# Kernel optimization log

Measured on AMD Instinct MI355X. Metric: run time of the kernel, lower is better.

Reference implementation:

```python
import jax, jax.numpy as jnp
import numpy as np

N = 50000      # n_nodes
E = 800000     # edges (before self-loops)
IN = 128       # in_dim
HID = 32       # hidden_dim (per-head out channels)
HEADS = 4
EMB = 128      # embed_dim
LAYERS = 3
NEG_SLOPE = 0.2  # PyG GATv2 default leaky_relu slope


def _layer_norm(x, g, b):
    mu = jnp.mean(x, axis=-1, keepdims=True)
    var = jnp.var(x, axis=-1, keepdims=True)
    return g * (x - mu) / jnp.sqrt(var + 1e-5) + b


def _gatv2(h, src, dst, n, Wl, bl, Wr, br, att, bias):
    # GATv2Conv (PyG semantics, share_weights=False, concat=True).
    H, C = att.shape
    xl = (h @ Wl + bl).reshape(n, H, C)   # target (i) transform
    xr = (h @ Wr + br).reshape(n, H, C)   # source (j) transform
    x_i = xl[dst]                          # [Etot, H, C] gather
    x_j = xr[src]
    e = jax.nn.leaky_relu(x_i + x_j, NEG_SLOPE)
    logit = jnp.einsum('ehc,hc->eh', e, att)          # [Etot, H]
    # segment softmax over destination node (every node has a self-loop)
    m = jax.ops.segment_max(logit, dst, num_segments=n)
    ex = jnp.exp(logit - m[dst])
    den = jax.ops.segment_sum(ex, dst, num_segments=n)
    alpha = ex / (den[dst] + 1e-16)
    out = jax.ops.segment_sum(alpha[..., None] * x_j, dst, num_segments=n)
    return out.reshape(n, H * C) + bias


def setup_inputs() -> dict:
    key = jax.random.key(0)
    ks = iter(jax.random.split(key, 64))
    d = {}
    d['x'] = jax.random.normal(next(ks), (N, IN), jnp.float32)
    d['edge_index'] = jax.random.randint(next(ks), (2, E), 0, N, dtype=jnp.int64)

    def w(shape, fan):
        return jax.random.normal(next(ks), shape, jnp.float32) / np.float32(np.sqrt(fan))

    HC = HID * HEADS
    d['W_in'] = w((IN, HID), IN); d['b_in'] = jnp.zeros((HID,), jnp.float32)
    for i in range(LAYERS):
        ic = HID if i == 0 else HC
        d[f'Wl{i}'] = w((ic, HC), ic); d[f'bl{i}'] = jnp.zeros((HC,), jnp.float32)
        d[f'Wr{i}'] = w((ic, HC), ic); d[f'br{i}'] = jnp.zeros((HC,), jnp.float32)
        d[f'att{i}'] = w((HEADS, HID), HID)
        d[f'bo{i}'] = jnp.zeros((HC,), jnp.float32)
        d[f'g{i}'] = jnp.ones((HC,), jnp.float32)
        d[f'be{i}'] = jnp.zeros((HC,), jnp.float32)
    d['W_out'] = w((HC, EMB), HC); d['b_out'] = jnp.zeros((EMB,), jnp.float32)
    return d


def reference(x, edge_index, W_in, b_in,
              Wl0, bl0, Wr0, br0, att0, bo0, g0, be0,
              Wl1, bl1, Wr1, br1, att1, bo1, g1, be1,
              Wl2, bl2, Wr2, br2, att2, bo2, g2, be2,
              W_out, b_out):
    n = x.shape[0]
    loops = jnp.arange(n, dtype=edge_index.dtype)  # add_self_loops=True
    src = jnp.concatenate([edge_index[0], loops])
    dst = jnp.concatenate([edge_index[1], loops])

    h = jax.nn.gelu(x @ W_in + b_in, approximate=False)
    layers = [(Wl0, bl0, Wr0, br0, att0, bo0, g0, be0),
              (Wl1, bl1, Wr1, br1, att1, bo1, g1, be1),
              (Wl2, bl2, Wr2, br2, att2, bo2, g2, be2)]
    for (Wl, bl, Wr, br, att, bo, g, be) in layers:
        h_new = jax.nn.gelu(_layer_norm(_gatv2(h, src, dst, n, Wl, bl, Wr, br, att, bo), g, be), approximate=False)
        h = h + h_new if h.shape == h_new.shape else h_new  # dropout = identity (eval)
    out = h @ W_out + b_out
    norm = jnp.maximum(jnp.linalg.norm(out, axis=-1, keepdims=True), 1e-12)
    return out / norm
```

## Files before the change

kernel.cpp:

```cpp
#include <hip/hip_runtime.h>
#include <hip/hip_bf16.h>
#include <math.h>

#define N_NODES 50000
#define N_EDGES 800000
#define IN_DIM  128
#define HC_DIM  128
#define HID_C   32
#define SCAN_NB 196

typedef __attribute__((ext_vector_type(8))) short short8;
typedef __attribute__((ext_vector_type(4))) short short4v;
typedef __attribute__((ext_vector_type(4))) float f32x4;

__device__ __forceinline__ float gelu_f(float x){
    return 0.5f*x*(1.0f + erff(x*0.7071067811865475f));
}

__device__ __forceinline__ void split2(float f, short& h, short& l){
    __hip_bfloat16 bh = __float2bfloat16(f);
    float r = f - __bfloat162float(bh);
    __hip_bfloat16 blo = __float2bfloat16(r);
    h = *reinterpret_cast<short*>(&bh);
    l = *reinterpret_cast<short*>(&blo);
}

__global__ __launch_bounds__(256) void k_count(const int* __restrict__ dst, int* __restrict__ cnt){
    int e = blockIdx.x*256 + threadIdx.x;
    if(e<N_EDGES) atomicAdd(&cnt[dst[e]], 1);
}

__global__ __launch_bounds__(256) void k_scan1(const int* __restrict__ cnt, int* __restrict__ rowptr,
                                               int* __restrict__ part){
    __shared__ int sh[256];
    int t=threadIdx.x; int i=blockIdx.x*256+t;
    int v = (i<N_NODES)? cnt[i] : 0;
    sh[t]=v; __syncthreads();
    for(int off=1; off<256; off<<=1){
        int y = (t>=off)? sh[t-off] : 0;
        __syncthreads();
        sh[t] += y;
        __syncthreads();
    }
    if(i<N_NODES) rowptr[i] = sh[t]-v;
    if(t==255) part[blockIdx.x] = sh[255];
}

__global__ __launch_bounds__(256) void k_scan2(int* __restrict__ part){
    __shared__ int sh[256];
    int t=threadIdx.x;
    int v = (t<SCAN_NB)? part[t] : 0;
    sh[t]=v; __syncthreads();
    for(int off=1; off<256; off<<=1){
        int y=(t>=off)? sh[t-off]:0;
        __syncthreads();
        sh[t]+=y;
        __syncthreads();
    }
    if(t<SCAN_NB) part[t] = sh[t]-v;
}

__global__ __launch_bounds__(256) void k_scan3(int* __restrict__ rowptr, const int* __restrict__ part,
                                               int* __restrict__ cur){
    int t=threadIdx.x; int i=blockIdx.x*256+t;
    if(i<N_NODES){
        int v = rowptr[i] + part[blockIdx.x];
        rowptr[i]=v; cur[i]=v;
    }
    if(i==0) rowptr[N_NODES]=N_EDGES;
}

__global__ __launch_bounds__(256) void k_fill(const int* __restrict__ src, const int* __restrict__ dst,
                                              int* __restrict__ cur, int* __restrict__ col){
    int e = blockIdx.x*256+threadIdx.x;
    if(e<N_EDGES){
        int d = dst[e];
        int p = atomicAdd(&cur[d],1);
        col[p] = src[e];
    }
}

__global__ __launch_bounds__(256) void k_splitW(const float* __restrict__ W0, const float* __restrict__ W1,
                                                const float* __restrict__ W2, const float* __restrict__ W3,
                                                const float* __restrict__ W4, const float* __restrict__ W5,
                                                const float* __restrict__ W6, short* __restrict__ WT){
    int bx = blockIdx.x;
    int m, kc;
    if(bx < 2){ m = bx; kc = 0; }
    else { m = 2 + (bx-2)/4; kc = (bx-2)&3; }
    const float* src; int K; size_t off;
    switch(m){
        case 0: src=W0; K=32;  off=0;      break;
        case 1: src=W1; K=32;  off=8192;   break;
        case 2: src=W2; K=128; off=16384;  break;
        case 3: src=W3; K=128; off=49152;  break;
        case 4: src=W4; K=128; off=81920;  break;
        case 5: src=W5; K=128; off=114688; break;
        default:src=W6; K=128; off=147456; break;
    }
    short* hi = WT + off;
    short* lo = hi + (size_t)K*HC_DIM;
    #pragma unroll
    for(int i=0;i<16;i++){
        int idx = threadIdx.x + i*256;
        int k = kc*32 + (idx>>7);
        int n = idx & 127;
        float f = src[(size_t)k*HC_DIM + n];
        short h,l; split2(f,h,l);
        hi[(size_t)n*K + k] = h;
        lo[(size_t)n*K + k] = l;
    }
}

__global__ __launch_bounds__(256) void k_gemm_in(const float* __restrict__ x, const float* __restrict__ W,
                                                 const float* __restrict__ b, float* __restrict__ h,
                                                 short* __restrict__ hhi, short* __restrict__ hlo){
    int id = blockIdx.x*256+threadIdx.x;
    int r = id>>5, c = id&31;
    const float4* x4 = (const float4*)(x + (size_t)r*IN_DIM);
    float acc=0.f;
    #pragma unroll 8
    for(int k=0;k<IN_DIM/4;k++){
        float4 xv = x4[k];
        acc = fmaf(xv.x, W[(4*k  )*HID_C+c], acc);
        acc = fmaf(xv.y, W[(4*k+1)*HID_C+c], acc);
        acc = fmaf(xv.z, W[(4*k+2)*HID_C+c], acc);
        acc = fmaf(xv.w, W[(4*k+3)*HID_C+c], acc);
    }
    float v = gelu_f(acc + b[c]);
    h[(size_t)r*HID_C+c] = v;
    short hh,ll; split2(v,hh,ll);
    hhi[(size_t)r*HID_C+c] = hh;
    hlo[(size_t)r*HID_C+c] = ll;
}

template<int K, bool PAIR>
__global__ __launch_bounds__(256) void k_mfma(const short* __restrict__ Ahi, const short* __restrict__ Alo,
                                              const short* __restrict__ WTl, const float* __restrict__ bl,
                                              const short* __restrict__ WTr, const float* __restrict__ br,
                                              float* __restrict__ XL, float* __restrict__ XR){
    constexpr int KC  = 32;
    constexpr int LDS_K = KC + 8;
    constexpr int NCH = K / KC;
    __shared__ short As_hi[64*LDS_K], As_lo[64*LDS_K];
    __shared__ short Wlh[64*LDS_K],  Wll[64*LDS_K];
    __shared__ short Wrh[64*LDS_K],  Wrl[64*LDS_K];

    int t = threadIdx.x;
    int lane = t & 63, wave = t >> 6;
    int quad = lane >> 4, ml = lane & 15;
    int rbase = blockIdx.x * 64;
    int nbase = blockIdx.y * 64;

    const short* WTl_lo = WTl + (size_t)K*HC_DIM;
    const short* WTr_lo = PAIR ? (WTr + (size_t)K*HC_DIM) : nullptr;

    f32x4 accL[4], accR[4];
    #pragma unroll
    for(int i=0;i<4;i++){ accL[i] = (f32x4){0.f,0.f,0.f,0.f}; accR[i] = (f32x4){0.f,0.f,0.f,0.f}; }

    int r = t >> 2, seg = t & 3;
    int gr = rbase + r; if(gr >= N_NODES) gr = N_NODES-1;

    for(int c=0; c<NCH; c++){
        if(c) __syncthreads();
        size_t ka = (size_t)gr*K + c*KC + seg*8;
        *(short8*)(As_hi + r*LDS_K + seg*8) = *(const short8*)(Ahi + ka);
        *(short8*)(As_lo + r*LDS_K + seg*8) = *(const short8*)(Alo + ka);
        size_t kw = (size_t)(nbase + r)*K + c*KC + seg*8;
        *(short8*)(Wlh + r*LDS_K + seg*8) = *(const short8*)(WTl + kw);
        *(short8*)(Wll + r*LDS_K + seg*8) = *(const short8*)(WTl_lo + kw);
        if(PAIR){
            *(short8*)(Wrh + r*LDS_K + seg*8) = *(const short8*)(WTr + kw);
            *(short8*)(Wrl + r*LDS_K + seg*8) = *(const short8*)(WTr_lo + kw);
        }
        __syncthreads();

        int k0 = quad*8;
        short8 wlh = *(const short8*)(Wlh + (wave*16 + ml)*LDS_K + k0);
        short8 wll = *(const short8*)(Wll + (wave*16 + ml)*LDS_K + k0);
        short8 wrh, wrl;
        if(PAIR){
            wrh = *(const short8*)(Wrh + (wave*16 + ml)*LDS_K + k0);
            wrl = *(const short8*)(Wrl + (wave*16 + ml)*LDS_K + k0);
        }
        #pragma unroll
        for(int i=0;i<4;i++){
            short8 ah = *(const short8*)(As_hi + (16*i + ml)*LDS_K + k0);
            short8 al = *(const short8*)(As_lo + (16*i + ml)*LDS_K + k0);
            accL[i] = __builtin_amdgcn_mfma_f32_16x16x32_bf16(ah, wlh, accL[i], 0,0,0);
            accL[i] = __builtin_amdgcn_mfma_f32_16x16x32_bf16(ah, wll, accL[i], 0,0,0);
            accL[i] = __builtin_amdgcn_mfma_f32_16x16x32_bf16(al, wlh, accL[i], 0,0,0);
            if(PAIR){
                accR[i] = __builtin_amdgcn_mfma_f32_16x16x32_bf16(ah, wrh, accR[i], 0,0,0);
                accR[i] = __builtin_amdgcn_mfma_f32_16x16x32_bf16(ah, wrl, accR[i], 0,0,0);
                accR[i] = __builtin_amdgcn_mfma_f32_16x16x32_bf16(al, wrh, accR[i], 0,0,0);
            }
        }
    }

    int col = nbase + wave*16 + ml;
    float bL = bl[col];
    float bR = PAIR ? br[col] : 0.f;
    #pragma unroll
    for(int i=0;i<4;i++){
        int row0 = rbase + 16*i + quad*4;
        #pragma unroll
        for(int rr=0;rr<4;rr++){
            int grr = row0 + rr;
            if(grr < N_NODES){
                XL[(size_t)grr*HC_DIM + col] = accL[i][rr] + bL;
                if(PAIR) XR[(size_t)grr*HC_DIM + col] = accR[i][rr] + bR;
            }
        }
    }
}

__global__ __launch_bounds__(256) void k_rownorm(const float* __restrict__ tmp, float* __restrict__ out){
    int wave=threadIdx.x>>6, lane=threadIdx.x&63;
    int node = blockIdx.x*4+wave;
    float2 v = *(const float2*)(tmp + (size_t)node*HC_DIM + 2*lane);
    float ss = v.x*v.x + v.y*v.y;
    #pragma unroll
    for(int msk=1;msk<64;msk<<=1) ss += __shfl_xor(ss,msk);
    float inv = 1.0f / fmaxf(sqrtf(ss), 1e-12f);
    *(float2*)(out + (size_t)node*HC_DIM + 2*lane) = make_float2(v.x*inv, v.y*inv);
}

__global__ __launch_bounds__(256) void k_node(const float* __restrict__ XL, const float* __restrict__ XR,
    const int* __restrict__ rowptr, const int* __restrict__ colidx,
    const float* __restrict__ att, const float* __restrict__ bo,
    const float* __restrict__ gg, const float* __restrict__ be,
    const float* __restrict__ hold, float* __restrict__ hout,
    short* __restrict__ hi_out, short* __restrict__ lo_out)
{
    int wave=threadIdx.x>>6, lane=threadIdx.x&63;
    int node = blockIdx.x*4+wave;
    int cg = lane & 31, half = lane >> 5;
    int c4 = cg << 2;

    float4 xl = *(const float4*)(XL + (size_t)node*HC_DIM + c4);
    float4 av = *(const float4*)(att + c4);
    int beg = rowptr[node], end = rowptr[node+1];

    #define EDGE_LOGIT(xj, q) { \
        float u0 = xl.x + xj.x; u0 = (u0>0.f)?u0:0.2f*u0; \
        float u1 = xl.y + xj.y; u1 = (u1>0.f)?u1:0.2f*u1; \
        float u2 = xl.z + xj.z; u2 = (u2>0.f)?u2:0.2f*u2; \
        float u3 = xl.w + xj.w; u3 = (u3>0.f)?u3:0.2f*u3; \
        q = fmaf(u0,av.x, fmaf(u1,av.y, fmaf(u2,av.z, u3*av.w))); \
        q += __shfl_xor(q,1); q += __shfl_xor(q,2); q += __shfl_xor(q,4); }

    float4 xs = *(const float4*)(XR + (size_t)node*HC_DIM + c4);
    float qs; EDGE_LOGIT(xs, qs)
    float m, ls; float4 acc;
    if(half==0){ m = qs; ls = 1.f; acc = xs; }
    else       { m = -INFINITY; ls = 0.f; acc = make_float4(0.f,0.f,0.f,0.f); }

    int P = end - beg;
    int nb = P >> 3;
    int base = beg;
    for(int b=0; b<nb; b++, base += 8){
        int j0 = colidx[base     + half];
        int j1 = colidx[base + 2 + half];
        int j2 = colidx[base + 4 + half];
        int j3 = colidx[base + 6 + half];
        float4 x0 = *(const float4*)(XR + (size_t)j0*HC_DIM + c4);
        float4 x1 = *(const float4*)(XR + (size_t)j1*HC_DIM + c4);
        float4 x2 = *(const float4*)(XR + (size_t)j2*HC_DIM + c4);
        float4 x3 = *(const float4*)(XR + (size_t)j3*HC_DIM + c4);
        float q0,q1,q2,q3;
        EDGE_LOGIT(x0,q0) EDGE_LOGIT(x1,q1) EDGE_LOGIT(x2,q2) EDGE_LOGIT(x3,q3)
        float nm = fmaxf(m, fmaxf(fmaxf(q0,q1),fmaxf(q2,q3)));
        float sc = __expf(m-nm);
        float e0 = __expf(q0-nm), e1 = __expf(q1-nm);
        float e2 = __expf(q2-nm), e3 = __expf(q3-nm);
        ls = fmaf(ls, sc, (e0+e1)+(e2+e3));
        acc.x = fmaf(acc.x, sc, fmaf(e0,x0.x, fmaf(e1,x1.x, fmaf(e2,x2.x, e3*x3.x))));
        acc.y = fmaf(acc.y, sc, fmaf(e0,x0.y, fmaf(e1,x1.y, fmaf(e2,x2.y, e3*x3.y))));
        acc.z = fmaf(acc.z, sc, fmaf(e0,x0.z, fmaf(e1,x1.z, fmaf(e2,x2.z, e3*x3.z))));
        acc.w = fmaf(acc.w, sc, fmaf(e0,x0.w, fmaf(e1,x1.w, fmaf(e2,x2.w, e3*x3.w))));
        m = nm;
    }
    #pragma unroll
    for(int i=0;i<4;i++){
        int idx = base + 2*i + half;
        if(idx < end){
            int j = colidx[idx];
            float4 xj = *(const float4*)(XR + (size_t)j*HC_DIM + c4);
            float q; EDGE_LOGIT(xj, q)
            float nm = fmaxf(m, q);
            float sc = __expf(m-nm);
            float p  = __expf(q-nm);
            ls = fmaf(ls, sc, p);
            acc.x = fmaf(acc.x, sc, p*xj.x);
            acc.y = fmaf(acc.y, sc, p*xj.y);
            acc.z = fmaf(acc.z, sc, p*xj.z);
            acc.w = fmaf(acc.w, sc, p*xj.w);
            m = nm;
        }
    }
    #undef EDGE_LOGIT

    {
        float mo  = __shfl_xor(m, 32);
        float lso = __shfl_xor(ls, 32);
        float4 ao;
        ao.x = __shfl_xor(acc.x,32); ao.y = __shfl_xor(acc.y,32);
        ao.z = __shfl_xor(acc.z,32); ao.w = __shfl_xor(acc.w,32);
        float nm = fmaxf(m, mo);
        float s0 = __expf(m-nm), s1 = __expf(mo-nm);
        ls = ls*s0 + lso*s1;
        acc.x = acc.x*s0 + ao.x*s1;
        acc.y = acc.y*s0 + ao.y*s1;
        acc.z = acc.z*s0 + ao.z*s1;
        acc.w = acc.w*s0 + ao.w*s1;
    }

    float inv = 1.0f/ls;
    float4 bo4 = *(const float4*)(bo + c4);
    float o0 = fmaf(acc.x,inv,bo4.x), o1 = fmaf(acc.y,inv,bo4.y);
    float o2 = fmaf(acc.z,inv,bo4.z), o3 = fmaf(acc.w,inv,bo4.w);
    float s1v = (o0+o1)+(o2+o3);
    float s2v = fmaf(o0,o0, fmaf(o1,o1, fmaf(o2,o2, o3*o3)));
    #pragma unroll
    for(int msk=1;msk<32;msk<<=1){ s1v += __shfl_xor(s1v,msk); s2v += __shfl_xor(s2v,msk); }
    float mean = s1v*(1.f/128.f);
    float var  = s2v*(1.f/128.f) - mean*mean;
    float rstd = rsqrtf(var + 1e-5f);
    float4 g4  = *(const float4*)(gg + c4);
    float4 be4 = *(const float4*)(be + c4);
    float r0 = gelu_f(fmaf(g4.x*(o0-mean), rstd, be4.x));
    float r1 = gelu_f(fmaf(g4.y*(o1-mean), rstd, be4.y));
    float r2 = gelu_f(fmaf(g4.z*(o2-mean), rstd, be4.z));
    float r3 = gelu_f(fmaf(g4.w*(o3-mean), rstd, be4.w));
    if(hold){
        float4 hv = *(const float4*)(hold + (size_t)node*HC_DIM + c4);
        r0 += hv.x; r1 += hv.y; r2 += hv.z; r3 += hv.w;
    }
    if(half==0){
        *(float4*)(hout + (size_t)node*HC_DIM + c4) = make_float4(r0,r1,r2,r3);
        short4v vh, vl; short hh, ll;
        split2(r0,hh,ll); vh[0]=hh; vl[0]=ll;
        split2(r1,hh,ll); vh[1]=hh; vl[1]=ll;
        split2(r2,hh,ll); vh[2]=hh; vl[2]=ll;
        split2(r3,hh,ll); vh[3]=hh; vl[3]=ll;
        *(short4v*)(hi_out + (size_t)node*HC_DIM + c4) = vh;
        *(short4v*)(lo_out + (size_t)node*HC_DIM + c4) = vl;
    }
}

extern "C" void kernel_launch(void* const* d_in, const int* in_sizes, int n_in,
                              void* d_out, int out_size, void* d_ws, size_t ws_size,
                              hipStream_t stream)
{
    const float* x   = (const float*)d_in[0];
    const int*   ei  = (const int*)  d_in[1];
    const float* Win = (const float*)d_in[2];
    const float* bin = (const float*)d_in[3];
    const float *Wl[3], *bl[3], *Wr[3], *br[3], *att[3], *bo[3], *gg[3], *be[3];
    for(int i=0;i<3;i++){
        const int base = 4 + 8*i;
        Wl[i]=(const float*)d_in[base+0]; bl[i]=(const float*)d_in[base+1];
        Wr[i]=(const float*)d_in[base+2]; br[i]=(const float*)d_in[base+3];
        att[i]=(const float*)d_in[base+4]; bo[i]=(const float*)d_in[base+5];
        gg[i]=(const float*)d_in[base+6]; be[i]=(const float*)d_in[base+7];
    }
    const float* Wout=(const float*)d_in[28];
    const float* bout=(const float*)d_in[29];
    float* out = (float*)d_out;

    char* w = (char*)d_ws;
    float* hA = (float*)w;  w += (size_t)N_NODES*HC_DIM*4;
    float* hB = (float*)w;  w += (size_t)N_NODES*HC_DIM*4;
    float* XL = (float*)w;  w += (size_t)N_NODES*HC_DIM*4;
    float* XR = (float*)w;  w += (size_t)N_NODES*HC_DIM*4;
    short* hAhi = (short*)w; w += (size_t)N_NODES*HC_DIM*2;
    short* hAlo = (short*)w; w += (size_t)N_NODES*HC_DIM*2;
    short* hBhi = (short*)w; w += (size_t)N_NODES*HC_DIM*2;
    short* hBlo = (short*)w; w += (size_t)N_NODES*HC_DIM*2;
    short* WT   = (short*)w; w += (size_t)180224*2;
    int* rowptr = (int*)w;  w += (size_t)(N_NODES+2)*4;
    int* cursor = (int*)w;  w += (size_t)N_NODES*4;
    int* colidx = (int*)w;  w += (size_t)N_EDGES*4;
    int* part   = (int*)w;  w += 256*4;

    const int* srcp = ei;
    const int* dstp = ei + N_EDGES;

    const dim3 gemm_grid(782, 2);

    k_splitW<<<22,256,0,stream>>>(Wl[0],Wr[0],Wl[1],Wr[1],Wl[2],Wr[2],Wout, WT);
    const short* WTl0 = WT + 0;      const short* WTr0 = WT + 8192;
    const short* WTl1 = WT + 16384;  const short* WTr1 = WT + 49152;
    const short* WTl2 = WT + 81920;  const short* WTr2 = WT + 114688;
    const short* WTo  = WT + 147456;

    hipMemsetAsync(cursor, 0, (size_t)N_NODES*4, stream);
    k_count <<<3125,256, 0, stream>>>(dstp, cursor);
    k_scan1 <<<SCAN_NB,256,0,stream>>>(cursor, rowptr, part);
    k_scan2 <<<1,   256, 0, stream>>>(part);
    k_scan3 <<<SCAN_NB,256,0,stream>>>(rowptr, part, cursor);
    k_fill  <<<3125,256, 0, stream>>>(srcp, dstp, cursor, colidx);

    k_gemm_in<<<6250,256,0,stream>>>(x, Win, bin, hA, hAhi, hAlo);

    k_mfma<32,true><<<gemm_grid,256,0,stream>>>(hAhi, hAlo, WTl0, bl[0], WTr0, br[0], XL, XR);
    k_node<<<12500,256,0,stream>>>(XL,XR,rowptr,colidx,att[0],bo[0],gg[0],be[0],
                                   (const float*)nullptr, hB, hBhi, hBlo);

    k_mfma<128,true><<<gemm_grid,256,0,stream>>>(hBhi, hBlo, WTl1, bl[1], WTr1, br[1], XL, XR);
    k_node<<<12500,256,0,stream>>>(XL,XR,rowptr,colidx,att[1],bo[1],gg[1],be[1], hB, hA, hAhi, hAlo);

    k_mfma<128,true><<<gemm_grid,256,0,stream>>>(hAhi, hAlo, WTl2, bl[2], WTr2, br[2], XL, XR);
    k_node<<<12500,256,0,stream>>>(XL,XR,rowptr,colidx,att[2],bo[2],gg[2],be[2], hA, hB, hBhi, hBlo);

    k_mfma<128,false><<<gemm_grid,256,0,stream>>>(hBhi, hBlo, WTo, bout, nullptr, nullptr, XL, nullptr);
    k_rownorm<<<12500,256,0,stream>>>(XL, out);
}
```

Baseline: 572.4 us.

## Fuse setup into cooperative kernel, store XR in bf16, widen GEMM tile, fuse rownorm

Merges the CSR build (count, scan, fill), weight splitting and input GEMM into a single cooperative kernel that uses grid syncs, replacing about eight separate launches. The source-side projection XR is now stored as bf16, halving the bytes moved by the edge-gather in the node kernel at some cost in precision. The MFMA GEMM now covers all 128 output columns per block instead of two 64-column blocks, and the output projection folds the L2 row normalisation into its epilogue, removing a separate kernel. The cooperative kernel runs the scattered atomics and the scan on only 512 blocks.

```diff
diff --git a/kernel.cpp b/kernel.cpp
--- a/kernel.cpp
+++ b/kernel.cpp
@@ -1,6 +1,9 @@
 #include <hip/hip_runtime.h>
 #include <hip/hip_bf16.h>
+#include <hip/hip_cooperative_groups.h>
 #include <math.h>
+
+namespace cg = cooperative_groups;
 
 #define N_NODES 50000
 #define N_EDGES 800000
@@ -8,6 +11,7 @@
 #define HC_DIM  128
 #define HID_C   32
 #define SCAN_NB 196
+#define COOP_NB 512
 
 typedef __attribute__((ext_vector_type(8))) short short8;
 typedef __attribute__((ext_vector_type(4))) short short4v;
@@ -24,210 +28,243 @@
     h = *reinterpret_cast<short*>(&bh);
     l = *reinterpret_cast<short*>(&blo);
 }
-
-__global__ __launch_bounds__(256) void k_count(const int* __restrict__ dst, int* __restrict__ cnt){
-    int e = blockIdx.x*256 + threadIdx.x;
-    if(e<N_EDGES) atomicAdd(&cnt[dst[e]], 1);
-}
-
-__global__ __launch_bounds__(256) void k_scan1(const int* __restrict__ cnt, int* __restrict__ rowptr,
-                                               int* __restrict__ part){
+__device__ __forceinline__ unsigned short f2bf(float f){
+    __hip_bfloat16 b = __float2bfloat16(f);
+    return *reinterpret_cast<unsigned short*>(&b);
+}
+__device__ __forceinline__ float bf2f(unsigned short u){
+    return __uint_as_float(((unsigned)u)<<16);
+}
+
+struct SetupArgs {
+    const float* x; const float* Win; const float* bin;
+    float* h; short* hhi; short* hlo;
+    const int* src; const int* dst;
+    int* cursor; int* rowptr; int* part; int* colidx;
+    const float* W[7];
+    short* WT;
+};
+
+__global__ __launch_bounds__(256) void k_setup(SetupArgs a){
+    cg::grid_group grid = cg::this_grid();
     __shared__ int sh[256];
-    int t=threadIdx.x; int i=blockIdx.x*256+t;
-    int v = (i<N_NODES)? cnt[i] : 0;
-    sh[t]=v; __syncthreads();
-    for(int off=1; off<256; off<<=1){
-        int y = (t>=off)? sh[t-off] : 0;
-        __syncthreads();
-        sh[t] += y;
-        __syncthreads();
-    }
-    if(i<N_NODES) rowptr[i] = sh[t]-v;
-    if(t==255) part[blockIdx.x] = sh[255];
-}
-
-__global__ __launch_bounds__(256) void k_scan2(int* __restrict__ part){
-    __shared__ int sh[256];
-    int t=threadIdx.x;
-    int v = (t<SCAN_NB)? part[t] : 0;
-    sh[t]=v; __syncthreads();
-    for(int off=1; off<256; off<<=1){
-        int y=(t>=off)? sh[t-off]:0;
-        __syncthreads();
-        sh[t]+=y;
-        __syncthreads();
-    }
-    if(t<SCAN_NB) part[t] = sh[t]-v;
-}
-
-__global__ __launch_bounds__(256) void k_scan3(int* __restrict__ rowptr, const int* __restrict__ part,
-                                               int* __restrict__ cur){
-    int t=threadIdx.x; int i=blockIdx.x*256+t;
-    if(i<N_NODES){
-        int v = rowptr[i] + part[blockIdx.x];
-        rowptr[i]=v; cur[i]=v;
-    }
-    if(i==0) rowptr[N_NODES]=N_EDGES;
-}
-
-__global__ __launch_bounds__(256) void k_fill(const int* __restrict__ src, const int* __restrict__ dst,
-                                              int* __restrict__ cur, int* __restrict__ col){
-    int e = blockIdx.x*256+threadIdx.x;
-    if(e<N_EDGES){
-        int d = dst[e];
-        int p = atomicAdd(&cur[d],1);
-        col[p] = src[e];
-    }
-}
-
-__global__ __launch_bounds__(256) void k_splitW(const float* __restrict__ W0, const float* __restrict__ W1,
-                                                const float* __restrict__ W2, const float* __restrict__ W3,
-                                                const float* __restrict__ W4, const float* __restrict__ W5,
-                                                const float* __restrict__ W6, short* __restrict__ WT){
-    int bx = blockIdx.x;
-    int m, kc;
-    if(bx < 2){ m = bx; kc = 0; }
-    else { m = 2 + (bx-2)/4; kc = (bx-2)&3; }
-    const float* src; int K; size_t off;
-    switch(m){
-        case 0: src=W0; K=32;  off=0;      break;
-        case 1: src=W1; K=32;  off=8192;   break;
-        case 2: src=W2; K=128; off=16384;  break;
-        case 3: src=W3; K=128; off=49152;  break;
-        case 4: src=W4; K=128; off=81920;  break;
-        case 5: src=W5; K=128; off=114688; break;
-        default:src=W6; K=128; off=147456; break;
-    }
-    short* hi = WT + off;
-    short* lo = hi + (size_t)K*HC_DIM;
-    #pragma unroll
-    for(int i=0;i<16;i++){
-        int idx = threadIdx.x + i*256;
-        int k = kc*32 + (idx>>7);
-        int n = idx & 127;
-        float f = src[(size_t)k*HC_DIM + n];
+    int t = threadIdx.x;
+    int gtid = blockIdx.x*256 + t;
+    const int gsize = COOP_NB*256;
+
+    for(int i=gtid; i<N_NODES; i+=gsize) a.cursor[i]=0;
+    for(int widx=gtid; widx<90112; widx+=gsize){
+        int m, e;
+        if(widx<4096){ m=0; e=widx; }
+        else if(widx<8192){ m=1; e=widx-4096; }
+        else { m = 2+(widx-8192)/16384; e = (widx-8192)%16384; }
+        int K = (m<2)?32:128;
+        size_t off;
+        switch(m){
+            case 0: off=0; break;      case 1: off=8192; break;
+            case 2: off=16384; break;  case 3: off=49152; break;
+            case 4: off=81920; break;  case 5: off=114688; break;
+            default: off=147456; break;
+        }
+        int n = e & 127, k = e >> 7;
+        float f = a.W[m][(size_t)k*HC_DIM + n];
         short h,l; split2(f,h,l);
-        hi[(size_t)n*K + k] = h;
-        lo[(size_t)n*K + k] = l;
-    }
-}
-
-__global__ __launch_bounds__(256) void k_gemm_in(const float* __restrict__ x, const float* __restrict__ W,
-                                                 const float* __restrict__ b, float* __restrict__ h,
-                                                 short* __restrict__ hhi, short* __restrict__ hlo){
-    int id = blockIdx.x*256+threadIdx.x;
-    int r = id>>5, c = id&31;
-    const float4* x4 = (const float4*)(x + (size_t)r*IN_DIM);
-    float acc=0.f;
-    #pragma unroll 8
-    for(int k=0;k<IN_DIM/4;k++){
-        float4 xv = x4[k];
-        acc = fmaf(xv.x, W[(4*k  )*HID_C+c], acc);
-        acc = fmaf(xv.y, W[(4*k+1)*HID_C+c], acc);
-        acc = fmaf(xv.z, W[(4*k+2)*HID_C+c], acc);
-        acc = fmaf(xv.w, W[(4*k+3)*HID_C+c], acc);
-    }
-    float v = gelu_f(acc + b[c]);
-    h[(size_t)r*HID_C+c] = v;
-    short hh,ll; split2(v,hh,ll);
-    hhi[(size_t)r*HID_C+c] = hh;
-    hlo[(size_t)r*HID_C+c] = ll;
-}
-
-template<int K, bool PAIR>
+        a.WT[off + (size_t)n*K + k] = h;
+        a.WT[off + (size_t)K*HC_DIM + (size_t)n*K + k] = l;
+    }
+    for(int oid=gtid; oid<N_NODES*HID_C; oid+=gsize){
+        int r = oid>>5, c = oid&31;
+        const float4* x4 = (const float4*)(a.x + (size_t)r*IN_DIM);
+        float acc=0.f;
+        #pragma unroll 8
+        for(int k=0;k<IN_DIM/4;k++){
+            float4 xv = x4[k];
+            acc = fmaf(xv.x, a.Win[(4*k  )*HID_C+c], acc);
+            acc = fmaf(xv.y, a.Win[(4*k+1)*HID_C+c], acc);
+            acc = fmaf(xv.z, a.Win[(4*k+2)*HID_C+c], acc);
+            acc = fmaf(xv.w, a.Win[(4*k+3)*HID_C+c], acc);
+        }
+        float v = gelu_f(acc + a.bin[c]);
+        a.h[oid] = v;
+        short hh,ll; split2(v,hh,ll);
+        a.hhi[oid]=hh; a.hlo[oid]=ll;
+    }
+    grid.sync();
+    for(int e=gtid; e<N_EDGES; e+=gsize) atomicAdd(&a.cursor[a.dst[e]], 1);
+    grid.sync();
+    if(blockIdx.x < SCAN_NB){
+        int i = blockIdx.x*256 + t;
+        int v = (i<N_NODES)? a.cursor[i] : 0;
+        sh[t]=v; __syncthreads();
+        for(int off=1; off<256; off<<=1){
+            int y = (t>=off)? sh[t-off] : 0;
+            __syncthreads();
+            sh[t] += y;
+            __syncthreads();
+        }
+        if(i<N_NODES) a.rowptr[i] = sh[t]-v;
+        if(t==255) a.part[blockIdx.x] = sh[255];
+    }
+    grid.sync();
+    if(blockIdx.x==0){
+        int v = (t<SCAN_NB)? a.part[t] : 0;
+        sh[t]=v; __syncthreads();
+        for(int off=1; off<256; off<<=1){
+            int y = (t>=off)? sh[t-off] : 0;
+            __syncthreads();
+            sh[t] += y;
+            __syncthreads();
+        }
+        if(t<SCAN_NB) a.part[t] = sh[t]-v;
+    }
+    grid.sync();
+    if(blockIdx.x < SCAN_NB){
+        int i = blockIdx.x*256 + t;
+        if(i<N_NODES){
+            int v = a.rowptr[i] + a.part[blockIdx.x];
+            a.rowptr[i]=v; a.cursor[i]=v;
+        }
+        if(i==0) a.rowptr[N_NODES]=N_EDGES;
+    }
+    grid.sync();
+    for(int e=gtid; e<N_EDGES; e+=gsize){
+        int d = a.dst[e];
+        int p = atomicAdd(&a.cursor[d], 1);
+        a.colidx[p] = a.src[e];
+    }
+}
+
+template<int K, bool PAIR, bool NORM>
 __global__ __launch_bounds__(256) void k_mfma(const short* __restrict__ Ahi, const short* __restrict__ Alo,
                                               const short* __restrict__ WTl, const float* __restrict__ bl,
                                               const short* __restrict__ WTr, const float* __restrict__ br,
-                                              float* __restrict__ XL, float* __restrict__ XR){
-    constexpr int KC  = 32;
-    constexpr int LDS_K = KC + 8;
-    constexpr int NCH = K / KC;
+                                              float* __restrict__ XL, unsigned short* __restrict__ XR16){
+    constexpr int LDS_K = 40;
+    constexpr int NCH = K / 32;
     __shared__ short As_hi[64*LDS_K], As_lo[64*LDS_K];
-    __shared__ short Wlh[64*LDS_K],  Wll[64*LDS_K];
-    __shared__ short Wrh[64*LDS_K],  Wrl[64*LDS_K];
+    __shared__ short Bh0[128*LDS_K], Bl0[128*LDS_K];
+    __shared__ short Bh1[PAIR?128*LDS_K:1], Bl1[PAIR?128*LDS_K:1];
+    __shared__ float ssq[NORM?256:1];
 
     int t = threadIdx.x;
     int lane = t & 63, wave = t >> 6;
     int quad = lane >> 4, ml = lane & 15;
     int rbase = blockIdx.x * 64;
-    int nbase = blockIdx.y * 64;
 
     const short* WTl_lo = WTl + (size_t)K*HC_DIM;
     const short* WTr_lo = PAIR ? (WTr + (size_t)K*HC_DIM) : nullptr;
 
-    f32x4 accL[4], accR[4];
+    f32x4 accL[4][2], accR[4][2];
     #pragma unroll
-    for(int i=0;i<4;i++){ accL[i] = (f32x4){0.f,0.f,0.f,0.f}; accR[i] = (f32x4){0.f,0.f,0.f,0.f}; }
+    for(int i=0;i<4;i++)
+        #pragma unroll
+        for(int j=0;j<2;j++){ accL[i][j]=(f32x4){0,0,0,0}; accR[i][j]=(f32x4){0,0,0,0}; }
 
     int r = t >> 2, seg = t & 3;
     int gr = rbase + r; if(gr >= N_NODES) gr = N_NODES-1;
 
     for(int c=0; c<NCH; c++){
         if(c) __syncthreads();
-        size_t ka = (size_t)gr*K + c*KC + seg*8;
+        size_t ka = (size_t)gr*K + c*32 + seg*8;
         *(short8*)(As_hi + r*LDS_K + seg*8) = *(const short8*)(Ahi + ka);
         *(short8*)(As_lo + r*LDS_K + seg*8) = *(const short8*)(Alo + ka);
-        size_t kw = (size_t)(nbase + r)*K + c*KC + seg*8;
-        *(short8*)(Wlh + r*LDS_K + seg*8) = *(const short8*)(WTl + kw);
-        *(short8*)(Wll + r*LDS_K + seg*8) = *(const short8*)(WTl_lo + kw);
-        if(PAIR){
-            *(short8*)(Wrh + r*LDS_K + seg*8) = *(const short8*)(WTr + kw);
-            *(short8*)(Wrl + r*LDS_K + seg*8) = *(const short8*)(WTr_lo + kw);
+        #pragma unroll
+        for(int u=0; u<2; u++){
+            int uu = t + u*256;
+            int n = uu >> 2, sg = uu & 3;
+            size_t kw = (size_t)n*K + c*32 + sg*8;
+            *(short8*)(Bh0 + n*LDS_K + sg*8) = *(const short8*)(WTl + kw);
+            *(short8*)(Bl0 + n*LDS_K + sg*8) = *(const short8*)(WTl_lo + kw);
+            if(PAIR){
+                *(short8*)(Bh1 + n*LDS_K + sg*8) = *(const short8*)(WTr + kw);
+                *(short8*)(Bl1 + n*LDS_K + sg*8) = *(const short8*)(WTr_lo + kw);
+            }
         }
         __syncthreads();
 
         int k0 = quad*8;
-        short8 wlh = *(const short8*)(Wlh + (wave*16 + ml)*LDS_K + k0);
-        short8 wll = *(const short8*)(Wll + (wave*16 + ml)*LDS_K + k0);
-        short8 wrh, wrl;
-        if(PAIR){
-            wrh = *(const short8*)(Wrh + (wave*16 + ml)*LDS_K + k0);
-            wrl = *(const short8*)(Wrl + (wave*16 + ml)*LDS_K + k0);
-        }
+        short8 ah[4], al[4];
         #pragma unroll
         for(int i=0;i<4;i++){
-            short8 ah = *(const short8*)(As_hi + (16*i + ml)*LDS_K + k0);
-            short8 al = *(const short8*)(As_lo + (16*i + ml)*LDS_K + k0);
-            accL[i] = __builtin_amdgcn_mfma_f32_16x16x32_bf16(ah, wlh, accL[i], 0,0,0);
-            accL[i] = __builtin_amdgcn_mfma_f32_16x16x32_bf16(ah, wll, accL[i], 0,0,0);
-            accL[i] = __builtin_amdgcn_mfma_f32_16x16x32_bf16(al, wlh, accL[i], 0,0,0);
+            ah[i] = *(const short8*)(As_hi + (16*i + ml)*LDS_K + k0);
+            al[i] = *(const short8*)(As_lo + (16*i + ml)*LDS_K + k0);
+        }
+        #pragma unroll
+        for(int j=0;j<2;j++){
+            int nrow = j*64 + wave*16 + ml;
+            short8 bh = *(const short8*)(Bh0 + nrow*LDS_K + k0);
+            short8 blo = *(const short8*)(Bl0 + nrow*LDS_K + k0);
+            #pragma unroll
+            for(int i=0;i<4;i++){
+                accL[i][j] = __builtin_amdgcn_mfma_f32_16x16x32_bf16(ah[i], bh,  accL[i][j], 0,0,0);
+                accL[i][j] = __builtin_amdgcn_mfma_f32_16x16x32_bf16(ah[i], blo, accL[i][j], 0,0,0);
+                accL[i][j] = __builtin_amdgcn_mfma_f32_16x16x32_bf16(al[i], bh,  accL[i][j], 0,0,0);
+            }
             if(PAIR){
-                accR[i] = __builtin_amdgcn_mfma_f32_16x16x32_bf16(ah, wrh, accR[i], 0,0,0);
-                accR[i] = __builtin_amdgcn_mfma_f32_16x16x32_bf16(ah, wrl, accR[i], 0,0,0);
-                accR[i] = __builtin_amdgcn_mfma_f32_16x16x32_bf16(al, wrh, accR[i], 0,0,0);
-            }
-        }
-    }
-
-    int col = nbase + wave*16 + ml;
-    float bL = bl[col];
-    float bR = PAIR ? br[col] : 0.f;
-    #pragma unroll
-    for(int i=0;i<4;i++){
-        int row0 = rbase + 16*i + quad*4;
-        #pragma unroll
-        for(int rr=0;rr<4;rr++){
-            int grr = row0 + rr;
-            if(grr < N_NODES){
-                XL[(size_t)grr*HC_DIM + col] = accL[i][rr] + bL;
-                if(PAIR) XR[(size_t)grr*HC_DIM + col] = accR[i][rr] + bR;
-            }
-        }
-    }
-}
-
-__global__ __launch_bounds__(256) void k_rownorm(const float* __restrict__ tmp, float* __restrict__ out){
-    int wave=threadIdx.x>>6, lane=threadIdx.x&63;
-    int node = blockIdx.x*4+wave;
-    float2 v = *(const float2*)(tmp + (size_t)node*HC_DIM + 2*lane);
-    float ss = v.x*v.x + v.y*v.y;
-    #pragma unroll
-    for(int msk=1;msk<64;msk<<=1) ss += __shfl_xor(ss,msk);
-    float inv = 1.0f / fmaxf(sqrtf(ss), 1e-12f);
-    *(float2*)(out + (size_t)node*HC_DIM + 2*lane) = make_float2(v.x*inv, v.y*inv);
-}
-
-__global__ __launch_bounds__(256) void k_node(const float* __restrict__ XL, const float* __restrict__ XR,
+                short8 ch = *(const short8*)(Bh1 + nrow*LDS_K + k0);
+                short8 cl = *(const short8*)(Bl1 + nrow*LDS_K + k0);
+                #pragma unroll
+                for(int i=0;i<4;i++){
+                    accR[i][j] = __builtin_amdgcn_mfma_f32_16x16x32_bf16(ah[i], ch, accR[i][j], 0,0,0);
+                    accR[i][j] = __builtin_amdgcn_mfma_f32_16x16x32_bf16(ah[i], cl, accR[i][j], 0,0,0);
+                    accR[i][j] = __builtin_amdgcn_mfma_f32_16x16x32_bf16(al[i], ch, accR[i][j], 0,0,0);
+                }
+            }
+        }
+    }
+
+    int col0 = wave*16 + ml, col1 = 64 + wave*16 + ml;
+    float bL0 = bl[col0], bL1 = bl[col1];
+
+    if(NORM){
+        #pragma unroll
+        for(int i=0;i<4;i++){
+            #pragma unroll
+            for(int rr=0;rr<4;rr++){
+                float v0 = accL[i][0][rr] + bL0;
+                float v1 = accL[i][1][rr] + bL1;
+                float p = v0*v0 + v1*v1;
+                p += __shfl_xor(p,1); p += __shfl_xor(p,2);
+                p += __shfl_xor(p,4); p += __shfl_xor(p,8);
+                if(ml==0) ssq[wave*64 + 16*i + quad*4 + rr] = p;
+            }
+        }
+        __syncthreads();
+        #pragma unroll
+        for(int i=0;i<4;i++){
+            #pragma unroll
+            for(int rr=0;rr<4;rr++){
+                int row = 16*i + quad*4 + rr;
+                int grr = rbase + row;
+                if(grr < N_NODES){
+                    float tot = ssq[row] + ssq[64+row] + ssq[128+row] + ssq[192+row];
+                    float inv = 1.0f / fmaxf(sqrtf(tot), 1e-12f);
+                    XL[(size_t)grr*HC_DIM + col0] = (accL[i][0][rr] + bL0) * inv;
+                    XL[(size_t)grr*HC_DIM + col1] = (accL[i][1][rr] + bL1) * inv;
+                }
+            }
+        }
+    } else {
+        float bR0 = PAIR ? br[col0] : 0.f, bR1 = PAIR ? br[col1] : 0.f;
+        #pragma unroll
+        for(int i=0;i<4;i++){
+            #pragma unroll
+            for(int rr=0;rr<4;rr++){
+                int grr = rbase + 16*i + quad*4 + rr;
+                if(grr < N_NODES){
+                    XL[(size_t)grr*HC_DIM + col0] = accL[i][0][rr] + bL0;
+                    XL[(size_t)grr*HC_DIM + col1] = accL[i][1][rr] + bL1;
+                    if(PAIR){
+                        XR16[(size_t)grr*HC_DIM + col0] = f2bf(accR[i][0][rr] + bR0);
+                        XR16[(size_t)grr*HC_DIM + col1] = f2bf(accR[i][1][rr] + bR1);
+                    }
+                }
+            }
+        }
+    }
+}
+
+__global__ __launch_bounds__(256) void k_node(const float* __restrict__ XL, const unsigned short* __restrict__ XR,
     const int* __restrict__ rowptr, const int* __restrict__ colidx,
     const float* __restrict__ att, const float* __restrict__ bo,
     const float* __restrict__ gg, const float* __restrict__ be,
@@ -243,6 +280,8 @@
     float4 av = *(const float4*)(att + c4);
     int beg = rowptr[node], end = rowptr[node+1];
 
+    #define LOADX(j, xx) { ushort4 u_ = *(const ushort4*)(XR + (size_t)(j)*HC_DIM + c4); \
+        xx = make_float4(bf2f(u_.x), bf2f(u_.y), bf2f(u_.z), bf2f(u_.w)); }
     #define EDGE_LOGIT(xj, q) { \
         float u0 = xl.x + xj.x; u0 = (u0>0.f)?u0:0.2f*u0; \
         float u1 = xl.y + xj.y; u1 = (u1>0.f)?u1:0.2f*u1; \
@@ -251,7 +290,7 @@
         q = fmaf(u0,av.x, fmaf(u1,av.y, fmaf(u2,av.z, u3*av.w))); \
         q += __shfl_xor(q,1); q += __shfl_xor(q,2); q += __shfl_xor(q,4); }
 
-    float4 xs = *(const float4*)(XR + (size_t)node*HC_DIM + c4);
+    float4 xs; LOADX(node, xs)
     float qs; EDGE_LOGIT(xs, qs)
     float m, ls; float4 acc;
     if(half==0){ m = qs; ls = 1.f; acc = xs; }
@@ -265,10 +304,8 @@
         int j1 = colidx[base + 2 + half];
         int j2 = colidx[base + 4 + half];
         int j3 = colidx[base + 6 + half];
-        float4 x0 = *(const float4*)(XR + (size_t)j0*HC_DIM + c4);
-        float4 x1 = *(const float4*)(XR + (size_t)j1*HC_DIM + c4);
-        float4 x2 = *(const float4*)(XR + (size_t)j2*HC_DIM + c4);
-        float4 x3 = *(const float4*)(XR + (size_t)j3*HC_DIM + c4);
+        float4 x0, x1, x2, x3;
+        LOADX(j0, x0) LOADX(j1, x1) LOADX(j2, x2) LOADX(j3, x3)
         float q0,q1,q2,q3;
         EDGE_LOGIT(x0,q0) EDGE_LOGIT(x1,q1) EDGE_LOGIT(x2,q2) EDGE_LOGIT(x3,q3)
         float nm = fmaxf(m, fmaxf(fmaxf(q0,q1),fmaxf(q2,q3)));
@@ -287,7 +324,7 @@
         int idx = base + 2*i + half;
         if(idx < end){
             int j = colidx[idx];
-            float4 xj = *(const float4*)(XR + (size_t)j*HC_DIM + c4);
+            float4 xj; LOADX(j, xj)
             float q; EDGE_LOGIT(xj, q)
             float nm = fmaxf(m, q);
             float sc = __expf(m-nm);
@@ -301,6 +338,7 @@
         }
     }
     #undef EDGE_LOGIT
+    #undef LOADX
 
     {
         float mo  = __shfl_xor(m, 32);
@@ -374,7 +412,7 @@
     float* hA = (float*)w;  w += (size_t)N_NODES*HC_DIM*4;
     float* hB = (float*)w;  w += (size_t)N_NODES*HC_DIM*4;
     float* XL = (float*)w;  w += (size_t)N_NODES*HC_DIM*4;
-    float* XR = (float*)w;  w += (size_t)N_NODES*HC_DIM*4;
+    unsigned short* XR16 = (unsigned short*)w; w += (size_t)N_NODES*HC_DIM*2;
     short* hAhi = (short*)w; w += (size_t)N_NODES*HC_DIM*2;
     short* hAlo = (short*)w; w += (size_t)N_NODES*HC_DIM*2;
     short* hBhi = (short*)w; w += (size_t)N_NODES*HC_DIM*2;
@@ -385,36 +423,31 @@
     int* colidx = (int*)w;  w += (size_t)N_EDGES*4;
     int* part   = (int*)w;  w += 256*4;
 
-    const int* srcp = ei;
-    const int* dstp = ei + N_EDGES;
-
-    const dim3 gemm_grid(782, 2);
-
-    k_splitW<<<22,256,0,stream>>>(Wl[0],Wr[0],Wl[1],Wr[1],Wl[2],Wr[2],Wout, WT);
     const short* WTl0 = WT + 0;      const short* WTr0 = WT + 8192;
     const short* WTl1 = WT + 16384;  const short* WTr1 = WT + 49152;
     const short* WTl2 = WT + 81920;  const short* WTr2 = WT + 114688;
     const short* WTo  = WT + 147456;
 
-    hipMemsetAsync(cursor, 0, (size_t)N_NODES*4, stream);
-    k_count <<<3125,256, 0, stream>>>(dstp, cursor);
-    k_scan1 <<<SCAN_NB,256,0,stream>>>(cursor, rowptr, part);
-    k_scan2 <<<1,   256, 0, stream>>>(part);
-    k_scan3 <<<SCAN_NB,256,0,stream>>>(rowptr, part, cursor);
-    k_fill  <<<3125,256, 0, stream>>>(srcp, dstp, cursor, colidx);
-
-    k_gemm_in<<<6250,256,0,stream>>>(x, Win, bin, hA, hAhi, hAlo);
-
-    k_mfma<32,true><<<gemm_grid,256,0,stream>>>(hAhi, hAlo, WTl0, bl[0], WTr0, br[0], XL, XR);
-    k_node<<<12500,256,0,stream>>>(XL,XR,rowptr,colidx,att[0],bo[0],gg[0],be[0],
+    SetupArgs sa;
+    sa.x = x; sa.Win = Win; sa.bin = bin;
+    sa.h = hA; sa.hhi = hAhi; sa.hlo = hAlo;
+    sa.src = ei; sa.dst = ei + N_EDGES;
+    sa.cursor = cursor; sa.rowptr = rowptr; sa.part = part; sa.colidx = colidx;
+    sa.W[0]=Wl[0]; sa.W[1]=Wr[0]; sa.W[2]=Wl[1]; sa.W[3]=Wr[1];
+    sa.W[4]=Wl[2]; sa.W[5]=Wr[2]; sa.W[6]=Wout;
+    sa.WT = WT;
+    void* kargs[] = { (void*)&sa };
+    hipLaunchCooperativeKernel((void*)k_setup, dim3(COOP_NB), dim3(256), kargs, 0, stream);
+
+    k_mfma<32,true,false><<<782,256,0,stream>>>(hAhi, hAlo, WTl0, bl[0], WTr0, br[0], XL, XR16);
+    k_node<<<12500,256,0,stream>>>(XL,XR16,rowptr,colidx,att[0],bo[0],gg[0],be[0],
                                    (const float*)nullptr, hB, hBhi, hBlo);
 
-    k_mfma<128,true><<<gemm_grid,256,0,stream>>>(hBhi, hBlo, WTl1, bl[1], WTr1, br[1], XL, XR);
-    k_node<<<12500,256,0,stream>>>(XL,XR,rowptr,colidx,att[1],bo[1],gg[1],be[1], hB, hA, hAhi, hAlo);
-
-    k_mfma<128,true><<<gemm_grid,256,0,stream>>>(hAhi, hAlo, WTl2, bl[2], WTr2, br[2], XL, XR);
-    k_node<<<12500,256,0,stream>>>(XL,XR,rowptr,colidx,att[2],bo[2],gg[2],be[2], hA, hB, hBhi, hBlo);
-
-    k_mfma<128,false><<<gemm_grid,256,0,stream>>>(hBhi, hBlo, WTo, bout, nullptr, nullptr, XL, nullptr);
-    k_rownorm<<<12500,256,0,stream>>>(XL, out);
-}
+    k_mfma<128,true,false><<<782,256,0,stream>>>(hBhi, hBlo, WTl1, bl[1], WTr1, br[1], XL, XR16);
+    k_node<<<12500,256,0,stream>>>(XL,XR16,rowptr,colidx,att[1],bo[1],gg[1],be[1], hB, hA, hAhi, hAlo);
+
+    k_mfma<128,true,false><<<782,256,0,stream>>>(hAhi, hAlo, WTl2, bl[2], WTr2, br[2], XL, XR16);
+    k_node<<<12500,256,0,stream>>>(XL,XR16,rowptr,colidx,att[2],bo[2],gg[2],be[2], hA, hB, hBhi, hBlo);
+
+    k_mfma<128,false,true><<<782,256,0,stream>>>(hBhi, hBlo, WTo, bout, nullptr, nullptr, out, nullptr);
+}
```

Result: slower. 826.7 us (+44.4%).
